# Kernel tuning notes

Measured on AMD Instinct MI355X. Metric: run time of the kernel, lower is better.

Reference implementation:

```python
import jax, jax.numpy as jnp
import numpy as np

T, B, D, H = 128, 256, 1024, 150  # seq_len, batch, input feat, lstm hidden (bidir out = 2H = 300)


def _lstm_dir(x, Wih, Whh, b):
    # x: [T,Bn,in]; Wih: [4H,in]; Whh: [4H,H]; b: [4H]. PyTorch gate order i,f,g,o.
    xW = jnp.einsum('tbi,gi->tbg', x, Wih) + b
    Bn = x.shape[1]
    init = (jnp.zeros((Bn, H), x.dtype), jnp.zeros((Bn, H), x.dtype))
    def step(carry, xg):
        h, c = carry
        g = xg + h @ Whh.T
        i, f, gg, o = jnp.split(g, 4, axis=-1)
        c = jax.nn.sigmoid(f) * c + jax.nn.sigmoid(i) * jnp.tanh(gg)
        h = jax.nn.sigmoid(o) * jnp.tanh(c)
        return (h, c), h
    _, hs = jax.lax.scan(step, init, xW)
    return hs


def _bidir(x, Wih, Whh, b):
    fwd = _lstm_dir(x, Wih[0], Whh[0], b[0])
    bwd = _lstm_dir(x[::-1], Wih[1], Whh[1], b[1])[::-1]
    return jnp.concatenate([fwd, bwd], axis=-1)


def _bilstm2(x, Wih0, Whh0, b0, Wih1, Whh1, b1):
    # 2-layer bidirectional LSTM (eval mode, dropout off)
    h = _bidir(x, Wih0, Whh0, b0)
    return _bidir(h, Wih1, Whh1, b1)


def setup_inputs() -> dict:
    key = jax.random.key(0)
    ks = iter(jax.random.split(key, 32))
    U = jax.random.normal(next(ks), (T, B, D), jnp.float32)
    speaker = jax.random.randint(next(ks), (T, B), 0, 2)
    qmask = jax.nn.one_hot(speaker, 2, dtype=jnp.int32)  # [T,B,2] speaker one-hot
    umask = jnp.ones((T, B), jnp.float32)
    seq_lengths = jnp.full((B,), T, dtype=jnp.int32)
    def w(shape):
        return jax.random.normal(next(ks), shape, jnp.float32) * 0.05
    inp = dict(U=U, qmask=qmask, umask=umask, seq_lengths=seq_lengths)
    for pfx in ('rnn', 'pr'):
        inp[pfx + '_Wih0'] = w((2, 4 * H, D))
        inp[pfx + '_Whh0'] = w((2, 4 * H, H))
        inp[pfx + '_b0'] = w((2, 4 * H))
        inp[pfx + '_Wih1'] = w((2, 4 * H, 2 * H))
        inp[pfx + '_Whh1'] = w((2, 4 * H, H))
        inp[pfx + '_b1'] = w((2, 4 * H))
    return inp


def reference(U, qmask, umask, seq_lengths, rnn_Wih0, rnn_Whh0, rnn_b0, rnn_Wih1, rnn_Whh1, rnn_b1, pr_Wih0, pr_Whh0, pr_b0, pr_Wih1, pr_Whh1, pr_b1):
    speaker = jnp.argmax(qmask, axis=-1)  # [T,B] party id of each utterance
    # position of utterance t within its party's compacted sequence
    pos = jnp.take_along_axis(jnp.cumsum(qmask, axis=0), speaker[..., None], axis=-1)[..., 0] - 1  # [T,B]
    bidx = jnp.broadcast_to(jnp.arange(B)[None, :], (T, B))
    # scatter utterances into per-party sequences: [2,T,B,D]
    U_parties = jnp.zeros((2, T, B, D), U.dtype).at[speaker, pos, bidx].set(U)
    xp = jnp.concatenate([U_parties[0], U_parties[1]], axis=1)  # [T,2B,D]
    Ep = _bilstm2(xp, pr_Wih0, pr_Whh0, pr_b0, pr_Wih1, pr_Whh1, pr_b1)  # [T,2B,2H]
    Ep = jnp.stack([Ep[:, :B], Ep[:, B:]], axis=0)  # [2,T,B,2H]
    U_p = Ep[speaker, pos, bidx]  # gather back to dialogue order, [T,B,2H]
    emotions = _bilstm2(U, rnn_Wih0, rnn_Whh0, rnn_b0, rnn_Wih1, rnn_Whh1, rnn_b1)  # [T,B,2H]
    return (emotions + U_p) * umask[..., None]
```

## Files before the change

kernel.cpp:

```cpp
#include <hip/hip_runtime.h>
#include <hip/hip_bf16.h>
#include <math.h>

#define T_ 128
#define B_ 256
#define BP 512
#define D_ 1024
#define H_ 150
#define G_ 600
#define O_ 300
#define ROWS 16
#define NT_ 38
#define KT_ 5
#define HSTR 168
#define GST 620
#define TPB 512
#define EIT 5
#define NTB 38

typedef float v4f    __attribute__((ext_vector_type(4)));
typedef short bf16x8 __attribute__((ext_vector_type(8)));
typedef float f32x4  __attribute__((ext_vector_type(4)));
typedef unsigned int u32x4 __attribute__((ext_vector_type(4)));
union HU { u32x4 u; bf16x8 h; };

static const size_t N_INV   = 0;
static const size_t N_WPK   = 65536;
static const size_t N_BPK   = N_WPK + 778240;
static const size_t N_HREG  = N_BPK + 2490368;
static const size_t N_X     = N_HREG + 29491200;
static const size_t N_TOTAL = N_X + 78643200 + 256;

static const size_t BPK0_STR = 1245184;
static const size_t BPK1_STR = 389120;

static const size_t INV_OFF   = 0;
static const size_t WIHT0_OFF = 65536;
static const size_t WIHT1_OFF = WIHT0_OFF + 4ull * 1024 * 600;
static const size_t WPK_OFF   = WIHT1_OFF + 4ull * 300 * 600;
static const size_t WPK_WORDS = 8ull * NT_ * KT_ * 2 * 512 / 2;
static const size_t XW_OFF    = WPK_OFF + WPK_WORDS;
static const size_t XSLOT     = 32768ull * 600;
static size_t hrnn_off(int nslots) { return XW_OFF + (size_t)nslots * XSLOT; }
static size_t hpr_off(int nslots)  { return hrnn_off(nslots) + 32768ull * 300; }
static size_t total_words(int nslots) { return hpr_off(nslots) + 65536ull * 300; }

__device__ __forceinline__ float fsig(float x) {
    return __builtin_amdgcn_rcpf(1.f + __expf(-x));
}
__device__ __forceinline__ float ftanh(float x) {
    float xc = fminf(fmaxf(x, -15.f), 15.f);
    float e = __expf(-2.f * xc);
    return (1.f - e) * __builtin_amdgcn_rcpf(1.f + e);
}

__global__ void k_pos(const int* __restrict__ qmask, int* __restrict__ inv) {
    int b = threadIdx.x;
    for (int p = 0; p < T_; ++p) {
        inv[p * BP + b] = -1;
        inv[p * BP + B_ + b] = -1;
    }
    int c0 = 0, c1 = 0;
    for (int t = 0; t < T_; ++t) {
        int s = qmask[(t * B_ + b) * 2 + 1];
        int p = s ? c1++ : c0++;
        inv[p * BP + s * B_ + b] = t * B_ + b;
    }
}

__global__ void k_transpose(const float* __restrict__ src, float* __restrict__ dst,
                            int K) {
    int idx = blockIdx.x * 256 + threadIdx.x;
    int total = K * G_;
    if (idx < total) {
        int k = idx / G_, g = idx - k * G_;
        dst[idx] = src[(size_t)g * K + k];
    }
}

struct PackArgs { const float* whh[8]; };
__global__ void k_pack(PackArgs pa, unsigned short* __restrict__ wpk) {
    int gid = blockIdx.x * 256 + threadIdx.x;
    int lane = gid & 63;
    int q = gid >> 6;
    int kt = q % KT_; q /= KT_;
    int nt = q % NT_; q /= NT_;
    if (q >= 8) return;
    const float* W = pa.whh[q];
    int col = nt * 16 + (lane & 15);
    int kbase = kt * 32 + (lane >> 4) * 8;
    size_t base = ((((size_t)q * NT_ + nt) * KT_ + kt) * 2) * 512 + (size_t)lane * 8;
    for (int j = 0; j < 8; ++j) {
        int k = kbase + j;
        float v = (col < G_ && k < H_) ? W[(size_t)col * H_ + k] : 0.f;
        unsigned u = __float_as_uint(v);
        unsigned short hi = (unsigned short)(u >> 16);
        float hf = __uint_as_float(u & 0xffff0000u);
        unsigned short lo = (unsigned short)(__float_as_uint(v - hf) >> 16);
        wpk[base + j] = hi;
        wpk[base + 512 + j] = lo;
    }
}

__global__ void k_packB(const float* __restrict__ W, int K, int KT,
                        unsigned short* __restrict__ out) {
    int gid = blockIdx.x * 256 + threadIdx.x;
    int lane = gid & 63, q = gid >> 6;
    int kt = q % KT, nt = q / KT;
    if (nt >= NTB) return;
    int col = nt * 16 + (lane & 15);
    int kb = kt * 32 + (lane >> 4) * 8;
    size_t base = ((size_t)(kt * NTB + nt) * 2) * 512 + (size_t)lane * 8;
    bf16x8 h8 = {0, 0, 0, 0, 0, 0, 0, 0};
    bf16x8 l8 = {0, 0, 0, 0, 0, 0, 0, 0};
#pragma unroll
    for (int j = 0; j < 8; ++j) {
        int k = kb + j;
        float v = (col < G_ && k < K) ? W[(size_t)col * K + k] : 0.f;
        unsigned u = __float_as_uint(v);
        h8[j] = (short)(u >> 16);
        float hf = __uint_as_float(u & 0xffff0000u);
        l8[j] = (short)(__float_as_uint(v - hf) >> 16);
    }
    *(bf16x8*)(out + base) = h8;
    *(bf16x8*)(out + base + 512) = l8;
}

__global__ void k_packU(const float* __restrict__ A, unsigned short* __restrict__ hi,
                        unsigned short* __restrict__ lo) {
    int gid = blockIdx.x * 256 + threadIdx.x;
    int kc = gid & 127, rr = gid >> 7;
    const float* ap = A + (size_t)rr * 1024 + kc * 8;
    size_t off = ((size_t)((rr >> 4) * 128 + kc) * 16 + (rr & 15)) * 8;
    bf16x8 h8, l8;
#pragma unroll
    for (int j = 0; j < 8; ++j) {
        float v = ap[j];
        unsigned u = __float_as_uint(v);
        h8[j] = (short)(u >> 16);
        float hf = __uint_as_float(u & 0xffff0000u);
        l8[j] = (short)(__float_as_uint(v - hf) >> 16);
    }
    *(bf16x8*)(hi + off) = h8;
    *(bf16x8*)(lo + off) = l8;
}

__global__ void k_recode(unsigned int* __restrict__ p, int n4) {
    int gid = blockIdx.x * 256 + threadIdx.x;
    if (gid >= n4) return;
    u32x4 w = *(u32x4*)(p + (size_t)gid * 4);
#pragma unroll
    for (int j = 0; j < 4; ++j) {
        unsigned u = w[j];
        float v = __uint_as_float(u);
        float hf = __uint_as_float(u & 0xffff0000u);
        w[j] = (u & 0xffff0000u) | (__float_as_uint(v - hf) >> 16);
    }
    *(u32x4*)(p + (size_t)gid * 4) = w;
}


#define LOADK(kt_, S)                                                          \
  {                                                                            \
    if (MODE == 0) {                                                           \
      _Pragma("unroll") for (int mi = 0; mi < 4; ++mi) {                       \
        size_t aoff = ((size_t)((m0 >> 4) + mi) * KA + (kt_) * 4 + quad);      \
        aoff = (aoff * 16 + col16) * 8;                                        \
        a_h##S[mi] = *(const bf16x8*)(Ahi + aoff);                             \
        a_l##S[mi] = *(const bf16x8*)(Alo + aoff);                             \
      }                                                                        \
    } else {                                                                   \
      _Pragma("unroll") for (int mi = 0; mi < 4; ++mi) {                       \
        const unsigned int* ap =                                               \
            Aw + (size_t)(m0 + mi * 16 + col16) * KA + (kt_) * 32 + quad * 8;  \
        u32x4 w0 = *(const u32x4*)ap;                                          \
        u32x4 w1 = *(const u32x4*)(ap + 4);                                    \
        HU hh, ll;                                                             \
        hh.u.x = (w0.x >> 16) | (w0.y & 0xffff0000u);                          \
        hh.u.y = (w0.z >> 16) | (w0.w & 0xffff0000u);                          \
        hh.u.z = (w1.x >> 16) | (w1.y & 0xffff0000u);                          \
        hh.u.w = (w1.z >> 16) | (w1.w & 0xffff0000u);                          \
        ll.u.x = (w0.x & 0xffffu) | (w0.y << 16);                              \
        ll.u.y = (w0.z & 0xffffu) | (w0.w << 16);                              \
        ll.u.z = (w1.x & 0xffffu) | (w1.y << 16);                              \
        ll.u.w = (w1.z & 0xffffu) | (w1.w << 16);                              \
        a_h##S[mi] = hh.h;                                                     \
        a_l##S[mi] = ll.h;                                                     \
      }                                                                        \
    }                                                                          \
    _Pragma("unroll") for (int ni = 0; ni < 4; ++ni) {                         \
      if (bnv[ni]) {                                                           \
        size_t bo = ((size_t)((kt_) * NTB + nt0 + ni) * 2) * 512 + lane * 8;   \
        b_h##S[ni] = *(const bf16x8*)(Bpk + bo);                               \
        b_l##S[ni] = *(const bf16x8*)(Bpk + bo + 512);                         \
      }                                                                        \
    }                                                                          \
  }

#define MMK(S)                                                                 \
  _Pragma("unroll") for (int mi = 0; mi < 4; ++mi)                             \
    _Pragma("unroll") for (int ni = 0; ni < 4; ++ni) {                         \
      acc[mi][ni] = __builtin_amdgcn_mfma_f32_16x16x32_bf16(                   \
          a_h##S[mi], b_h##S[ni], acc[mi][ni], 0, 0, 0);                       \
      acc[mi][ni] = __builtin_amdgcn_mfma_f32_16x16x32_bf16(                   \
          a_h##S[mi], b_l##S[ni], acc[mi][ni], 0, 0, 0);                       \
      acc[mi][ni] = __builtin_amdgcn_mfma_f32_16x16x32_bf16(                   \
          a_l##S[mi], b_h##S[ni], acc[mi][ni], 0, 0, 0);                       \
    }

template<int MODE, int KTN, int KA>
__global__ __launch_bounds__(256) void k_mgemm(const unsigned short* __restrict__ Ahi,
                                               const unsigned short* __restrict__ Alo,
                                               const unsigned int* __restrict__ Aw,
                                               const unsigned short* __restrict__ Bpk,
                                               const float* __restrict__ bias,
                                               float* __restrict__ C) {
    int tid = threadIdx.x, lane = tid & 63, wv = tid >> 6;
    int col16 = lane & 15, quad = lane >> 4;
    int n0 = blockIdx.x * 128 + (wv & 1) * 64;
    int m0 = blockIdx.y * 128 + (wv >> 1) * 64;
    int nt0 = n0 >> 4;

    bool bnv[4]; float bs[4];
#pragma unroll
    for (int ni = 0; ni < 4; ++ni) {
        int nt = nt0 + ni;
        bnv[ni] = (nt < NTB);
        int cc = nt * 16 + col16;
        bs[ni] = (cc < G_) ? bias[cc] : 0.f;
    }

    f32x4 acc[4][4];
#pragma unroll
    for (int mi = 0; mi < 4; ++mi)
#pragma unroll
        for (int ni = 0; ni < 4; ++ni) acc[mi][ni] = (f32x4){0.f, 0.f, 0.f, 0.f};

    bf16x8 z8 = {0, 0, 0, 0, 0, 0, 0, 0};
    bf16x8 a_h0[4], a_l0[4], b_h0[4], b_l0[4];
    bf16x8 a_h1[4], a_l1[4], b_h1[4], b_l1[4];
#pragma unroll
    for (int ni = 0; ni < 4; ++ni) {
        b_h0[ni] = z8; b_l0[ni] = z8; b_h1[ni] = z8; b_l1[ni] = z8;
    }

    LOADK(0, 0);
#pragma unroll 1
    for (int kt = 0; kt < KTN; kt += 2) {
        LOADK(kt + 1, 1);
        MMK(0);
        if (kt + 2 < KTN) { LOADK(kt + 2, 0); }
        MMK(1);
    }

#pragma unroll
    for (int mi = 0; mi < 4; ++mi)
#pragma unroll
        for (int ni = 0; ni < 4; ++ni) {
            int col = n0 + ni * 16 + col16;
            if (col < G_) {
#pragma unroll
                for (int p = 0; p < 4; ++p)
                    C[(size_t)(m0 + mi * 16 + quad * 4 + p) * G_ + col] =
                        acc[mi][ni][p] + bs[ni];
            }
        }
}

__global__ __launch_bounds__(256) void k_gemm(const float* __restrict__ A,
                                              const float* __restrict__ BT,
                                              const float* __restrict__ bias,
                                              float* __restrict__ C,
                                              int M, int K) {
    __shared__ __align__(16) float As[16][136];
    __shared__ __align__(16) float Bs[16][68];
    int n0 = blockIdx.x * 64, m0 = blockIdx.y * 128;
    int tid = threadIdx.x;
    int tx = tid & 15, ty = tid >> 4;
    int ar = tid >> 2, ac = (tid & 3) * 4;
    int kr = tid >> 4, nc = (tid & 15) * 4;
    float acc[8][4];
#pragma unroll
    for (int i = 0; i < 8; ++i)
#pragma unroll
        for (int j = 0; j < 4; ++j) acc[i][j] = 0.f;

    for (int k0 = 0; k0 < K; k0 += 16) {
        bool fullK = (k0 + 16 <= K);
#pragma unroll
        for (int half = 0; half < 2; ++half) {
            int m = m0 + ar + half * 64;
            const float* ap = A + (size_t)m * K + k0 + ac;
            if (fullK) {
                v4f v = *(const v4f*)ap;
                As[ac + 0][ar + half * 64] = v.x;
                As[ac + 1][ar + half * 64] = v.y;
                As[ac + 2][ar + half * 64] = v.z;
                As[ac + 3][ar + half * 64] = v.w;
            } else {
#pragma unroll
                for (int i = 0; i < 4; ++i) {
                    int k = k0 + ac + i;
                    As[ac + i][ar + half * 64] = (k < K) ? ap[i] : 0.f;
                }
            }
        }
        {
            int k = k0 + kr, n = n0 + nc;
            if (fullK && n + 3 < G_) {
                v4f v = *(const v4f*)(BT + (size_t)k * G_ + n);
                Bs[kr][nc + 0] = v.x; Bs[kr][nc + 1] = v.y;
                Bs[kr][nc + 2] = v.z; Bs[kr][nc + 3] = v.w;
            } else {
#pragma unroll
                for (int i = 0; i < 4; ++i) {
                    int nn = n + i;
                    Bs[kr][nc + i] = (k < K && nn < G_) ? BT[(size_t)k * G_ + nn] : 0.f;
                }
            }
        }
        __syncthreads();
#pragma unroll
        for (int kk = 0; kk < 16; ++kk) {
            v4f a0 = *(const v4f*)&As[kk][ty * 8];
            v4f a1 = *(const v4f*)&As[kk][ty * 8 + 4];
            v4f b  = *(const v4f*)&Bs[kk][tx * 4];
            const float* af = (const float*)&a0;
            const float* af2 = (const float*)&a1;
            const float* bf = (const float*)&b;
#pragma unroll
            for (int i = 0; i < 4; ++i)
#pragma unroll
                for (int j = 0; j < 4; ++j) {
                    acc[i][j] += af[i] * bf[j];
                    acc[4 + i][j] += af2[i] * bf[j];
                }
        }
        __syncthreads();
    }
    int n = n0 + tx * 4;
    if (n + 3 < G_) {
        v4f bv = *(const v4f*)(bias + n);
#pragma unroll
        for (int i = 0; i < 8; ++i) {
            int m = m0 + ty * 8 + i;
            v4f o = {acc[i][0] + bv.x, acc[i][1] + bv.y, acc[i][2] + bv.z, acc[i][3] + bv.w};
            *(v4f*)(C + (size_t)m * G_ + n) = o;
        }
    } else {
#pragma unroll
        for (int i = 0; i < 8; ++i) {
            int m = m0 + ty * 8 + i;
#pragma unroll
            for (int j = 0; j < 4; ++j)
                if (n + j < G_) C[(size_t)m * G_ + n + j] = acc[i][j] + bias[n + j];
        }
    }
}

struct Combo {
    const float* xw;
    const unsigned short* wpk;
    const float* bias;
    float* out;
    int Bn, colOff, bwd, gIn, gOut;
};
struct ScanArgs {
    Combo c[4];
    const int* inv;
    const float* addSrc;
    const float* umask;
    int blkStart[5];
};

__global__ __launch_bounds__(TPB) void k_scan(ScanArgs args) {
    int bx = blockIdx.x, ci = 0;
#pragma unroll
    for (int i = 1; i < 4; ++i)
        if (bx >= args.blkStart[i]) ci = i;
    Combo cb = args.c[ci];
    int row0 = (bx - args.blkStart[ci]) * ROWS;

    __shared__ __align__(16) unsigned short hsh[ROWS * HSTR];
    __shared__ __align__(16) unsigned short hsl[ROWS * HSTR];
    __shared__ float cs[ROWS * 152];
    __shared__ float gs[ROWS * GST];
    int tid = threadIdx.x;
    int lane = tid & 63, wv = tid >> 6;
    int col16 = lane & 15, quad = lane >> 4;
    for (int i = tid; i < ROWS * HSTR; i += TPB) { hsh[i] = 0; hsl[i] = 0; }
    for (int i = tid; i < ROWS * 152; i += TPB) cs[i] = 0.f;
    __syncthreads();

    int er[EIT], ej[EIT];
#pragma unroll
    for (int it = 0; it < EIT; ++it) {
        int i = tid + it * TPB;
        er[it] = i / 160;
        ej[it] = i - er[it] * 160;
    }

    for (int s = 0; s < T_; ++s) {
        int t = cb.bwd ? (T_ - 1 - s) : s;

        float xi[EIT], xf_[EIT], xg[EIT], xo[EIT];
#pragma unroll
        for (int it = 0; it < EIT; ++it) {
            int r = er[it], j = ej[it];
            const float* xr;
            if (cb.gIn) {
                int g = args.inv[t * cb.Bn + row0 + r];
                xr = (g >= 0) ? cb.xw + (size_t)g * G_ : cb.bias;
            } else {
                xr = cb.xw + ((size_t)t * cb.Bn + row0 + r) * G_;
            }
            bool act = (j < H_);
            xi[it]  = act ? xr[j] : 0.f;
            xf_[it] = act ? xr[H_ + j] : 0.f;
            xg[it]  = act ? xr[2 * H_ + j] : 0.f;
            xo[it]  = act ? xr[3 * H_ + j] : 0.f;
        }

        bf16x8 ahi[KT_], alo[KT_];
#pragma unroll
        for (int kt = 0; kt < KT_; ++kt) {
            int off = col16 * HSTR + kt * 32 + quad * 8;
            ahi[kt] = *(const bf16x8*)&hsh[off];
            alo[kt] = *(const bf16x8*)&hsl[off];
        }

        for (int nt = wv; nt < NT_; nt += 8) {
            f32x4 a0 = {0.f, 0.f, 0.f, 0.f};
            f32x4 a1 = {0.f, 0.f, 0.f, 0.f};
            const bf16x8* bp = (const bf16x8*)cb.wpk + ((size_t)nt * KT_) * 2 * 64 + lane;
#pragma unroll
            for (int kt = 0; kt < KT_; ++kt) {
                bf16x8 bhi = bp[0];
                bf16x8 blo = bp[64];
                bp += 128;
                if (kt < 3) {
                    a0 = __builtin_amdgcn_mfma_f32_16x16x32_bf16(ahi[kt], bhi, a0, 0, 0, 0);
                    a0 = __builtin_amdgcn_mfma_f32_16x16x32_bf16(ahi[kt], blo, a0, 0, 0, 0);
                    a0 = __builtin_amdgcn_mfma_f32_16x16x32_bf16(alo[kt], bhi, a0, 0, 0, 0);
                } else {
                    a1 = __builtin_amdgcn_mfma_f32_16x16x32_bf16(ahi[kt], bhi, a1, 0, 0, 0);
                    a1 = __builtin_amdgcn_mfma_f32_16x16x32_bf16(ahi[kt], blo, a1, 0, 0, 0);
                    a1 = __builtin_amdgcn_mfma_f32_16x16x32_bf16(alo[kt], bhi, a1, 0, 0, 0);
                }
            }
            f32x4 acc = a0 + a1;
#pragma unroll
            for (int p = 0; p < 4; ++p)
                gs[(quad * 4 + p) * GST + nt * 16 + col16] = acc[p];
        }
        __syncthreads();

#pragma unroll
        for (int it = 0; it < EIT; ++it) {
            int r = er[it], j = ej[it];
            if (j < H_) {
                float gi = gs[r * GST + j] + xi[it];
                float gf = gs[r * GST + H_ + j] + xf_[it];
                float gg = gs[r * GST + 2 * H_ + j] + xg[it];
                float go = gs[r * GST + 3 * H_ + j] + xo[it];
                float ii = fsig(gi), ff = fsig(gf), oo = fsig(go);
                float cc = ff * cs[r * 152 + j] + ii * ftanh(gg);
                float hh = oo * ftanh(cc);
                cs[r * 152 + j] = cc;
                unsigned u = __float_as_uint(hh);
                hsh[r * HSTR + j] = (unsigned short)(u >> 16);
                float hf = __uint_as_float(u & 0xffff0000u);
                hsl[r * HSTR + j] = (unsigned short)(__float_as_uint(hh - hf) >> 16);
                if (cb.gOut) {
                    int g = args.inv[t * cb.Bn + row0 + r];
                    if (g >= 0) {
                        size_t o = (size_t)g * O_ + cb.colOff + j;
                        if (args.addSrc)
                            cb.out[o] = (args.addSrc[o] + hh) * args.umask[g];
                        else
                            cb.out[o] = hh;
                    }
                } else {
                    cb.out[((size_t)t * cb.Bn + row0 + r) * O_ + cb.colOff + j] = hh;
                }
            }
        }
        __syncthreads();
    }
}

extern "C" void kernel_launch(void* const* d_in, const int* in_sizes, int n_in,
                              void* d_out, int out_size, void* d_ws, size_t ws_size,
                              hipStream_t stream) {
    const float* U        = (const float*)d_in[0];
    const int*   qmask    = (const int*)d_in[1];
    const float* umask    = (const float*)d_in[2];
    const float* rnn_Wih0 = (const float*)d_in[4];
    const float* rnn_Whh0 = (const float*)d_in[5];
    const float* rnn_b0   = (const float*)d_in[6];
    const float* rnn_Wih1 = (const float*)d_in[7];
    const float* rnn_Whh1 = (const float*)d_in[8];
    const float* rnn_b1   = (const float*)d_in[9];
    const float* pr_Wih0  = (const float*)d_in[10];
    const float* pr_Whh0  = (const float*)d_in[11];
    const float* pr_b0    = (const float*)d_in[12];
    const float* pr_Wih1  = (const float*)d_in[13];
    const float* pr_Whh1  = (const float*)d_in[14];
    const float* pr_b1    = (const float*)d_in[15];

    float* ws = (float*)d_ws;
    dim3 blk(256);
    dim3 sblk(TPB);
    const int INF = 0x7fffffff;

    const size_t WPS = (size_t)NT_ * KT_ * 2 * 512;

    ScanArgs z = {};
    auto setCombo = [&](ScanArgs& sa, int i, const float* xw, unsigned short* wbase,
                        int wslot, const float* bi, float* o, int Bn, int co, int bw,
                        int gi, int go) {
        sa.c[i].xw = xw; sa.c[i].wpk = wbase + (size_t)wslot * WPS;
        sa.c[i].bias = bi; sa.c[i].out = o;
        sa.c[i].Bn = Bn; sa.c[i].colOff = co; sa.c[i].bwd = bw;
        sa.c[i].gIn = gi; sa.c[i].gOut = go;
    };

    PackArgs pa;
    for (int d = 0; d < 2; ++d) {
        pa.whh[0 + d] = rnn_Whh0 + (size_t)d * G_ * H_;
        pa.whh[2 + d] = pr_Whh0  + (size_t)d * G_ * H_;
        pa.whh[4 + d] = rnn_Whh1 + (size_t)d * G_ * H_;
        pa.whh[6 + d] = pr_Whh1  + (size_t)d * G_ * H_;
    }
    int packLanes = 8 * NT_ * KT_ * 64;

    if (ws_size >= N_TOTAL * 4ull) {
        int*   inv   = (int*)d_ws + N_INV;
        unsigned short* wpk = (unsigned short*)(ws + N_WPK);
        unsigned short* bpk = (unsigned short*)(ws + N_BPK);
        float* h_rnn = ws + N_HREG;
        float* h_pr  = h_rnn + 32768ull * 300;
        unsigned short* Uhi = (unsigned short*)h_rnn;
        unsigned short* Ulo = Uhi + 16384ull * 1024;
        float* X[4];
        for (int i = 0; i < 4; ++i) X[i] = ws + N_X + (size_t)i * 19660800ull;

        k_pos<<<dim3(1), dim3(256), 0, stream>>>(qmask, inv);
        k_pack<<<dim3((packLanes + 255) / 256), dim3(256), 0, stream>>>(pa, wpk);

        const float* W0p[4] = {rnn_Wih0, rnn_Wih0 + (size_t)G_ * D_,
                               pr_Wih0,  pr_Wih0 + (size_t)G_ * D_};
        const float* b0p[4] = {rnn_b0, rnn_b0 + G_, pr_b0, pr_b0 + G_};
        {
            int lanes = 32 * NTB * 64;
            for (int g = 0; g < 4; ++g)
                k_packB<<<dim3((lanes + 255) / 256), blk, 0, stream>>>(
                    W0p[g], D_, 32, bpk + (size_t)g * BPK0_STR);
        }

        dim3 gm0(5, 128);
        for (int half = 0; half < 2; ++half) {
            k_packU<<<dim3(8192), blk, 0, stream>>>(U + (size_t)half * 16384 * D_, Uhi, Ulo);
            for (int g = 0; g < 4; ++g)
                k_mgemm<0, 32, 128><<<gm0, blk, 0, stream>>>(
                    Uhi, Ulo, nullptr, bpk + (size_t)g * BPK0_STR, b0p[g],
                    X[g] + (size_t)half * 16384 * G_);
        }

        ScanArgs sa = z;
        sa.inv = inv;
        setCombo(sa, 0, X[0], wpk, 0, nullptr, h_rnn, B_, 0, 0, 0, 0);
        setCombo(sa, 1, X[1], wpk, 1, nullptr, h_rnn, B_, H_, 1, 0, 0);
        setCombo(sa, 2, X[2], wpk, 2, pr_b0 + 0 * G_, h_pr, BP, 0, 0, 1, 0);
        setCombo(sa, 3, X[3], wpk, 3, pr_b0 + 1 * G_, h_pr, BP, H_, 1, 1, 0);
        sa.blkStart[0] = 0; sa.blkStart[1] = 16; sa.blkStart[2] = 32;
        sa.blkStart[3] = 64; sa.blkStart[4] = 96;
        k_scan<<<dim3(96), sblk, 0, stream>>>(sa);

        k_recode<<<dim3((2457600 + 255) / 256), blk, 0, stream>>>((unsigned int*)h_rnn, 2457600);
        k_recode<<<dim3((4915200 + 255) / 256), blk, 0, stream>>>((unsigned int*)h_pr, 4915200);
        const float* W1p[4] = {rnn_Wih1, rnn_Wih1 + (size_t)G_ * O_,
                               pr_Wih1,  pr_Wih1 + (size_t)G_ * O_};
        {
            int lanes = 10 * NTB * 64;
            for (int g = 0; g < 4; ++g)
                k_packB<<<dim3((lanes + 255) / 256), blk, 0, stream>>>(
                    W1p[g], O_, 10, bpk + (size_t)g * BPK1_STR);
        }

        dim3 gm1r(5, 256), gm1p(5, 512);
        k_mgemm<1, 10, 300><<<gm1r, blk, 0, stream>>>(
            nullptr, nullptr, (unsigned int*)h_rnn, bpk + 0 * BPK1_STR, rnn_b1 + 0 * G_, X[0]);
        k_mgemm<1, 10, 300><<<gm1r, blk, 0, stream>>>(
            nullptr, nullptr, (unsigned int*)h_rnn, bpk + 1 * BPK1_STR, rnn_b1 + 1 * G_, X[1]);
        k_mgemm<1, 10, 300><<<gm1p, blk, 0, stream>>>(
            nullptr, nullptr, (unsigned int*)h_pr, bpk + 2 * BPK1_STR, pr_b1 + 0 * G_, X[2]);
        ScanArgs sr = z;
        sr.inv = inv;
        setCombo(sr, 0, X[0], wpk, 4, nullptr, h_rnn, B_, 0, 0, 0, 0);
        setCombo(sr, 1, X[1], wpk, 5, nullptr, h_rnn, B_, H_, 1, 0, 0);
        sr.blkStart[0] = 0; sr.blkStart[1] = 16; sr.blkStart[2] = INF;
        sr.blkStart[3] = INF; sr.blkStart[4] = 32;
        k_scan<<<dim3(32), sblk, 0, stream>>>(sr);

        k_mgemm<1, 10, 300><<<gm1p, blk, 0, stream>>>(
            nullptr, nullptr, (unsigned int*)h_pr, bpk + 3 * BPK1_STR, pr_b1 + 1 * G_, X[0]);
        ScanArgs sp = z;
        sp.inv = inv; sp.addSrc = h_rnn; sp.umask = umask;
        setCombo(sp, 0, X[2], wpk, 6, nullptr, (float*)d_out, BP, 0, 0, 0, 1);
        setCombo(sp, 1, X[0], wpk, 7, nullptr, (float*)d_out, BP, H_, 1, 0, 1);
        sp.blkStart[0] = 0; sp.blkStart[1] = 32; sp.blkStart[2] = INF;
        sp.blkStart[3] = INF; sp.blkStart[4] = 64;
        k_scan<<<dim3(64), sblk, 0, stream>>>(sp);
        return;
    }

    int*   inv   = (int*)d_ws + INV_OFF;
    float* wihT0 = ws + WIHT0_OFF;
    float* wihT1 = ws + WIHT1_OFF;
    unsigned short* wpk = (unsigned short*)(ws + WPK_OFF);
    float* X0    = ws + XW_OFF;
    float* X1    = X0 + XSLOT;
    float* h_rnn = ws + hrnn_off(2);
    float* h_pr  = ws + hpr_off(2);

    const size_t W0S = 1024ull * 600, W1S = 300ull * 600;

    k_pos<<<dim3(1), dim3(256), 0, stream>>>(qmask, inv);
    auto TP = [&](const float* src, float* dst, int K) {
        int total = K * G_;
        k_transpose<<<dim3((total + 255) / 256), dim3(256), 0, stream>>>(src, dst, K);
    };
    for (int d = 0; d < 2; ++d) {
        TP(rnn_Wih0 + (size_t)d * G_ * D_, wihT0 + (0 + d) * W0S, D_);
        TP(pr_Wih0  + (size_t)d * G_ * D_, wihT0 + (2 + d) * W0S, D_);
        TP(rnn_Wih1 + (size_t)d * G_ * O_, wihT1 + (0 + d) * W1S, O_);
        TP(pr_Wih1  + (size_t)d * G_ * O_, wihT1 + (2 + d) * W1S, O_);
    }
    k_pack<<<dim3((packLanes + 255) / 256), dim3(256), 0, stream>>>(pa, wpk);

    dim3 g32k(10, 256), g64k(10, 512);
    for (int d = 0; d < 2; ++d) {
        k_gemm<<<g32k, blk, 0, stream>>>(U, wihT0 + (0 + d) * W0S, rnn_b0 + d * G_, X0, 32768, D_);
        k_gemm<<<g32k, blk, 0, stream>>>(U, wihT0 + (2 + d) * W0S, pr_b0 + d * G_, X1, 32768, D_);
        ScanArgs sa = z;
        sa.inv = inv;
        setCombo(sa, 0, X0, wpk, 0 + d, nullptr, h_rnn, B_, d * H_, d, 0, 0);
        setCombo(sa, 1, X1, wpk, 2 + d, pr_b0 + d * G_, h_pr, BP, d * H_, d, 1, 0);
        sa.blkStart[0] = 0; sa.blkStart[1] = 16; sa.blkStart[2] = INF;
        sa.blkStart[3] = INF; sa.blkStart[4] = 48;
        k_scan<<<dim3(48), sblk, 0, stream>>>(sa);
    }
    k_gemm<<<g32k, blk, 0, stream>>>(h_rnn, wihT1 + 0 * W1S, rnn_b1 + 0 * G_, X0, 32768, O_);
    k_gemm<<<g32k, blk, 0, stream>>>(h_rnn, wihT1 + 1 * W1S, rnn_b1 + 1 * G_, X1, 32768, O_);
    {
        ScanArgs sr = z;
        sr.inv = inv;
        setCombo(sr, 0, X0, wpk, 4, nullptr, h_rnn, B_, 0, 0, 0, 0);
        setCombo(sr, 1, X1, wpk, 5, nullptr, h_rnn, B_, H_, 1, 0, 0);
        sr.blkStart[0] = 0; sr.blkStart[1] = 16; sr.blkStart[2] = INF;
        sr.blkStart[3] = INF; sr.blkStart[4] = 32;
        k_scan<<<dim3(32), sblk, 0, stream>>>(sr);
    }
    for (int d = 0; d < 2; ++d) {
        k_gemm<<<g64k, blk, 0, stream>>>(h_pr, wihT1 + (2 + d) * W1S, pr_b1 + d * G_, X0, 65536, O_);
        ScanArgs sp = z;
        sp.inv = inv; sp.addSrc = h_rnn; sp.umask = umask;
        setCombo(sp, 0, X0, wpk, 6 + d, nullptr, (float*)d_out, BP, d * H_, d, 0, 1);
        sp.blkStart[0] = 0; sp.blkStart[1] = INF; sp.blkStart[2] = INF;
        sp.blkStart[3] = INF; sp.blkStart[4] = 32;
        k_scan<<<dim3(32), sblk, 0, stream>>>(sp);
    }
}
```

Measured before the change: 4.103 ms.

## Fuse layer-1 input projection into recurrent scan and run all four layer-1 scans concurrently

Layer 0 now writes its hidden states straight into a packed bf16 hi/lo MFMA operand layout, so the separate recode pass goes away. Layer 1 no longer runs a separate input-projection GEMM. Each timestep of the new scan kernel computes x·Wih with MFMA alongside h·Whh. This lets all four layer-1 direction/stack scans run in one 96-block launch instead of two serialized launches, and the final residual add plus mask becomes a separate elementwise kernel. The trade-off is extra per-step MFMA and global loads of Wih inside the latency-bound recurrence, plus a zeroing pass over the packed buffer.

```diff
diff --git a/kernel.cpp b/kernel.cpp
--- a/kernel.cpp
+++ b/kernel.cpp
@@ -12,6 +12,8 @@
 #define ROWS 16
 #define NT_ 38
 #define KT_ 5
+#define KTX 10
+#define KAP 40
 #define HSTR 168
 #define GST 620
 #define TPB 512
@@ -26,13 +28,16 @@
 
 static const size_t N_INV   = 0;
 static const size_t N_WPK   = 65536;
-static const size_t N_BPK   = N_WPK + 778240;
-static const size_t N_HREG  = N_BPK + 2490368;
-static const size_t N_X     = N_HREG + 29491200;
+static const size_t N_BW1   = N_WPK + 778240;
+static const size_t N_HPK   = N_BW1 + 778240;
+static const size_t N_X     = N_HPK + 31457280;
 static const size_t N_TOTAL = N_X + 78643200 + 256;
 
-static const size_t BPK0_STR = 1245184;
-static const size_t BPK1_STR = 389120;
+static const size_t WPS      = (size_t)NT_ * KT_ * 2 * 512;
+static const size_t BW1_STR  = (size_t)KTX * NTB * 2 * 512;
+static const size_t BW0_STR  = 32ull * NTB * 2 * 512;
+static const size_t RNN_PL   = 2048ull * KAP * 128;
+static const size_t PR_PL    = 4096ull * KAP * 128;
 
 static const size_t INV_OFF   = 0;
 static const size_t WIHT0_OFF = 65536;
@@ -43,7 +48,6 @@
 static const size_t XSLOT     = 32768ull * 600;
 static size_t hrnn_off(int nslots) { return XW_OFF + (size_t)nslots * XSLOT; }
 static size_t hpr_off(int nslots)  { return hrnn_off(nslots) + 32768ull * 300; }
-static size_t total_words(int nslots) { return hpr_off(nslots) + 65536ull * 300; }
 
 __device__ __forceinline__ float fsig(float x) {
     return __builtin_amdgcn_rcpf(1.f + __expf(-x));
@@ -66,6 +70,11 @@
         int p = s ? c1++ : c0++;
         inv[p * BP + s * B_ + b] = t * B_ + b;
     }
+}
+
+__global__ void k_zero(unsigned int* __restrict__ p, int n4) {
+    int gid = blockIdx.x * 256 + threadIdx.x;
+    if (gid < n4) *(u32x4*)(p + (size_t)gid * 4) = (u32x4){0, 0, 0, 0};
 }
 
 __global__ void k_transpose(const float* __restrict__ src, float* __restrict__ dst,
@@ -144,21 +153,6 @@
     *(bf16x8*)(hi + off) = h8;
     *(bf16x8*)(lo + off) = l8;
 }
-
-__global__ void k_recode(unsigned int* __restrict__ p, int n4) {
-    int gid = blockIdx.x * 256 + threadIdx.x;
-    if (gid >= n4) return;
-    u32x4 w = *(u32x4*)(p + (size_t)gid * 4);
-#pragma unroll
-    for (int j = 0; j < 4; ++j) {
-        unsigned u = w[j];
-        float v = __uint_as_float(u);
-        float hf = __uint_as_float(u & 0xffff0000u);
-        w[j] = (u & 0xffff0000u) | (__float_as_uint(v - hf) >> 16);
-    }
-    *(u32x4*)(p + (size_t)gid * 4) = w;
-}
-
 
 #define LOADK(kt_, S)                                                          \
   {                                                                            \
@@ -358,6 +352,269 @@
     }
 }
 
+struct Combo0 {
+    const float* xw;
+    const unsigned short* wpk;
+    const float* bias;
+    unsigned short* phi;
+    unsigned short* plo;
+    int Bn, colOff, bwd, gIn;
+};
+struct Scan0Args { Combo0 c[4]; const int* inv; int blkStart[5]; };
+
+__global__ __launch_bounds__(TPB) void k_scan0(Scan0Args args) {
+    int bx = blockIdx.x, ci = 0;
+#pragma unroll
+    for (int i = 1; i < 4; ++i)
+        if (bx >= args.blkStart[i]) ci = i;
+    Combo0 cb = args.c[ci];
+    int row0 = (bx - args.blkStart[ci]) * ROWS;
+
+    __shared__ __align__(16) unsigned short hsh[ROWS * HSTR];
+    __shared__ __align__(16) unsigned short hsl[ROWS * HSTR];
+    __shared__ float cs[ROWS * 152];
+    __shared__ float gs[ROWS * GST];
+    int tid = threadIdx.x;
+    int lane = tid & 63, wv = tid >> 6;
+    int col16 = lane & 15, quad = lane >> 4;
+    for (int i = tid; i < ROWS * HSTR; i += TPB) { hsh[i] = 0; hsl[i] = 0; }
+    for (int i = tid; i < ROWS * 152; i += TPB) cs[i] = 0.f;
+    __syncthreads();
+
+    int er[EIT], ej[EIT];
+#pragma unroll
+    for (int it = 0; it < EIT; ++it) {
+        int i = tid + it * TPB;
+        er[it] = i / 160;
+        ej[it] = i - er[it] * 160;
+    }
+
+    for (int s = 0; s < T_; ++s) {
+        int t = cb.bwd ? (T_ - 1 - s) : s;
+
+        float xi[EIT], xf_[EIT], xg[EIT], xo[EIT];
+#pragma unroll
+        for (int it = 0; it < EIT; ++it) {
+            int r = er[it], j = ej[it];
+            const float* xr;
+            if (cb.gIn) {
+                int g = args.inv[t * cb.Bn + row0 + r];
+                xr = (g >= 0) ? cb.xw + (size_t)g * G_ : cb.bias;
+            } else {
+                xr = cb.xw + ((size_t)t * cb.Bn + row0 + r) * G_;
+            }
+            bool act = (j < H_);
+            xi[it]  = act ? xr[j] : 0.f;
+            xf_[it] = act ? xr[H_ + j] : 0.f;
+            xg[it]  = act ? xr[2 * H_ + j] : 0.f;
+            xo[it]  = act ? xr[3 * H_ + j] : 0.f;
+        }
+
+        bf16x8 ahi[KT_], alo[KT_];
+#pragma unroll
+        for (int kt = 0; kt < KT_; ++kt) {
+            int off = col16 * HSTR + kt * 32 + quad * 8;
+            ahi[kt] = *(const bf16x8*)&hsh[off];
+            alo[kt] = *(const bf16x8*)&hsl[off];
+        }
+
+        for (int nt = wv; nt < NT_; nt += 8) {
+            f32x4 a0 = {0.f, 0.f, 0.f, 0.f};
+            f32x4 a1 = {0.f, 0.f, 0.f, 0.f};
+            const bf16x8* bp = (const bf16x8*)cb.wpk + ((size_t)nt * KT_) * 2 * 64 + lane;
+#pragma unroll
+            for (int kt = 0; kt < KT_; ++kt) {
+                bf16x8 bhi = bp[0];
+                bf16x8 blo = bp[64];
+                bp += 128;
+                if (kt < 3) {
+                    a0 = __builtin_amdgcn_mfma_f32_16x16x32_bf16(ahi[kt], bhi, a0, 0, 0, 0);
+                    a0 = __builtin_amdgcn_mfma_f32_16x16x32_bf16(ahi[kt], blo, a0, 0, 0, 0);
+                    a0 = __builtin_amdgcn_mfma_f32_16x16x32_bf16(alo[kt], bhi, a0, 0, 0, 0);
+                } else {
+                    a1 = __builtin_amdgcn_mfma_f32_16x16x32_bf16(ahi[kt], bhi, a1, 0, 0, 0);
+                    a1 = __builtin_amdgcn_mfma_f32_16x16x32_bf16(ahi[kt], blo, a1, 0, 0, 0);
+                    a1 = __builtin_amdgcn_mfma_f32_16x16x32_bf16(alo[kt], bhi, a1, 0, 0, 0);
+                }
+            }
+            f32x4 acc = a0 + a1;
+#pragma unroll
+            for (int p = 0; p < 4; ++p)
+                gs[(quad * 4 + p) * GST + nt * 16 + col16] = acc[p];
+        }
+        __syncthreads();
+
+        size_t mb = ((size_t)t * cb.Bn + row0) >> 4;
+#pragma unroll
+        for (int it = 0; it < EIT; ++it) {
+            int r = er[it], j = ej[it];
+            if (j < H_) {
+                float gi = gs[r * GST + j] + xi[it];
+                float gf = gs[r * GST + H_ + j] + xf_[it];
+                float gg = gs[r * GST + 2 * H_ + j] + xg[it];
+                float go = gs[r * GST + 3 * H_ + j] + xo[it];
+                float ii = fsig(gi), ff = fsig(gf), oo = fsig(go);
+                float cc = ff * cs[r * 152 + j] + ii * ftanh(gg);
+                float hh = oo * ftanh(cc);
+                cs[r * 152 + j] = cc;
+                unsigned u = __float_as_uint(hh);
+                unsigned short hi16 = (unsigned short)(u >> 16);
+                float hf = __uint_as_float(u & 0xffff0000u);
+                unsigned short lo16 = (unsigned short)(__float_as_uint(hh - hf) >> 16);
+                hsh[r * HSTR + j] = hi16;
+                hsl[r * HSTR + j] = lo16;
+                int k = cb.colOff + j;
+                size_t off = (mb * KAP + (k >> 3)) * 128 + (size_t)r * 8 + (k & 7);
+                cb.phi[off] = hi16;
+                cb.plo[off] = lo16;
+            }
+        }
+        __syncthreads();
+    }
+}
+
+struct Combo1 {
+    const unsigned short* xphi;
+    const unsigned short* xplo;
+    const unsigned short* whh;
+    const unsigned short* wih;
+    const float* bias;
+    float* out;
+    int Bn, colOff, bwd, gOut;
+};
+struct Scan1Args { Combo1 c[4]; const int* inv; int blkStart[5]; };
+
+__global__ __launch_bounds__(TPB) void k_scan1(Scan1Args args) {
+    int bx = blockIdx.x, ci = 0;
+#pragma unroll
+    for (int i = 1; i < 4; ++i)
+        if (bx >= args.blkStart[i]) ci = i;
+    Combo1 cb = args.c[ci];
+    int row0 = (bx - args.blkStart[ci]) * ROWS;
+
+    __shared__ __align__(16) unsigned short hsh[ROWS * HSTR];
+    __shared__ __align__(16) unsigned short hsl[ROWS * HSTR];
+    __shared__ float cs[ROWS * 152];
+    __shared__ float gs[ROWS * GST];
+    int tid = threadIdx.x;
+    int lane = tid & 63, wv = tid >> 6;
+    int col16 = lane & 15, quad = lane >> 4;
+    for (int i = tid; i < ROWS * HSTR; i += TPB) { hsh[i] = 0; hsl[i] = 0; }
+    for (int i = tid; i < ROWS * 152; i += TPB) cs[i] = 0.f;
+    __syncthreads();
+
+    int er[EIT], ej[EIT];
+    float bxi[EIT], bxf[EIT], bxg[EIT], bxo[EIT];
+#pragma unroll
+    for (int it = 0; it < EIT; ++it) {
+        int i = tid + it * TPB;
+        er[it] = i / 160;
+        ej[it] = i - er[it] * 160;
+        int j = ej[it];
+        bool act = (j < H_);
+        bxi[it] = act ? cb.bias[j] : 0.f;
+        bxf[it] = act ? cb.bias[H_ + j] : 0.f;
+        bxg[it] = act ? cb.bias[2 * H_ + j] : 0.f;
+        bxo[it] = act ? cb.bias[3 * H_ + j] : 0.f;
+    }
+
+    for (int s = 0; s < T_; ++s) {
+        int t = cb.bwd ? (T_ - 1 - s) : s;
+        size_t mb = ((size_t)t * cb.Bn + row0) >> 4;
+
+        bf16x8 xh[KTX], xl[KTX];
+#pragma unroll
+        for (int kt = 0; kt < KTX; ++kt) {
+            size_t off = (mb * KAP + kt * 4 + quad) * 128 + (size_t)col16 * 8;
+            xh[kt] = *(const bf16x8*)(cb.xphi + off);
+            xl[kt] = *(const bf16x8*)(cb.xplo + off);
+        }
+
+        bf16x8 ahi[KT_], alo[KT_];
+#pragma unroll
+        for (int kt = 0; kt < KT_; ++kt) {
+            int off = col16 * HSTR + kt * 32 + quad * 8;
+            ahi[kt] = *(const bf16x8*)&hsh[off];
+            alo[kt] = *(const bf16x8*)&hsl[off];
+        }
+
+        for (int nt = wv; nt < NT_; nt += 8) {
+            f32x4 a0 = {0.f, 0.f, 0.f, 0.f};
+            f32x4 a1 = {0.f, 0.f, 0.f, 0.f};
+            const bf16x8* bp = (const bf16x8*)cb.whh + ((size_t)nt * KT_) * 2 * 64 + lane;
+#pragma unroll
+            for (int kt = 0; kt < KT_; ++kt) {
+                bf16x8 bhi = bp[0];
+                bf16x8 blo = bp[64];
+                bp += 128;
+                if (kt < 3) {
+                    a0 = __builtin_amdgcn_mfma_f32_16x16x32_bf16(ahi[kt], bhi, a0, 0, 0, 0);
+                    a0 = __builtin_amdgcn_mfma_f32_16x16x32_bf16(ahi[kt], blo, a0, 0, 0, 0);
+                    a0 = __builtin_amdgcn_mfma_f32_16x16x32_bf16(alo[kt], bhi, a0, 0, 0, 0);
+                } else {
+                    a1 = __builtin_amdgcn_mfma_f32_16x16x32_bf16(ahi[kt], bhi, a1, 0, 0, 0);
+                    a1 = __builtin_amdgcn_mfma_f32_16x16x32_bf16(ahi[kt], blo, a1, 0, 0, 0);
+                    a1 = __builtin_amdgcn_mfma_f32_16x16x32_bf16(alo[kt], bhi, a1, 0, 0, 0);
+                }
+            }
+#pragma unroll
+            for (int kt = 0; kt < KTX; ++kt) {
+                const bf16x8* xp = (const bf16x8*)cb.wih + ((size_t)(kt * NTB + nt) * 2) * 64 + lane;
+                bf16x8 bhi = xp[0];
+                bf16x8 blo = xp[64];
+                if (kt & 1) {
+                    a1 = __builtin_amdgcn_mfma_f32_16x16x32_bf16(xh[kt], bhi, a1, 0, 0, 0);
+                    a1 = __builtin_amdgcn_mfma_f32_16x16x32_bf16(xh[kt], blo, a1, 0, 0, 0);
+                    a1 = __builtin_amdgcn_mfma_f32_16x16x32_bf16(xl[kt], bhi, a1, 0, 0, 0);
+                } else {
+                    a0 = __builtin_amdgcn_mfma_f32_16x16x32_bf16(xh[kt], bhi, a0, 0, 0, 0);
+                    a0 = __builtin_amdgcn_mfma_f32_16x16x32_bf16(xh[kt], blo, a0, 0, 0, 0);
+                    a0 = __builtin_amdgcn_mfma_f32_16x16x32_bf16(xl[kt], bhi, a0, 0, 0, 0);
+                }
+            }
+            f32x4 acc = a0 + a1;
+#pragma unroll
+            for (int p = 0; p < 4; ++p)
+                gs[(quad * 4 + p) * GST + nt * 16 + col16] = acc[p];
+        }
+        __syncthreads();
+
+#pragma unroll
+        for (int it = 0; it < EIT; ++it) {
+            int r = er[it], j = ej[it];
+            if (j < H_) {
+                float gi = gs[r * GST + j] + bxi[it];
+                float gf = gs[r * GST + H_ + j] + bxf[it];
+                float gg = gs[r * GST + 2 * H_ + j] + bxg[it];
+                float go = gs[r * GST + 3 * H_ + j] + bxo[it];
+                float ii = fsig(gi), ff = fsig(gf), oo = fsig(go);
+                float cc = ff * cs[r * 152 + j] + ii * ftanh(gg);
+                float hh = oo * ftanh(cc);
+                cs[r * 152 + j] = cc;
+                unsigned u = __float_as_uint(hh);
+                hsh[r * HSTR + j] = (unsigned short)(u >> 16);
+                float hf = __uint_as_float(u & 0xffff0000u);
+                hsl[r * HSTR + j] = (unsigned short)(__float_as_uint(hh - hf) >> 16);
+                if (cb.gOut) {
+                    int g = args.inv[t * cb.Bn + row0 + r];
+                    if (g >= 0)
+                        cb.out[(size_t)g * O_ + cb.colOff + j] = hh;
+                } else {
+                    cb.out[((size_t)t * cb.Bn + row0 + r) * O_ + cb.colOff + j] = hh;
+                }
+            }
+        }
+        __syncthreads();
+    }
+}
+
+__global__ void k_add(float* __restrict__ out, const float* __restrict__ up,
+                      const float* __restrict__ um) {
+    int idx = blockIdx.x * 256 + threadIdx.x;
+    if (idx < T_ * B_ * O_)
+        out[idx] = (out[idx] + up[idx]) * um[idx / O_];
+}
+
 struct Combo {
     const float* xw;
     const unsigned short* wpk;
@@ -513,18 +770,6 @@
     dim3 sblk(TPB);
     const int INF = 0x7fffffff;
 
-    const size_t WPS = (size_t)NT_ * KT_ * 2 * 512;
-
-    ScanArgs z = {};
-    auto setCombo = [&](ScanArgs& sa, int i, const float* xw, unsigned short* wbase,
-                        int wslot, const float* bi, float* o, int Bn, int co, int bw,
-                        int gi, int go) {
-        sa.c[i].xw = xw; sa.c[i].wpk = wbase + (size_t)wslot * WPS;
-        sa.c[i].bias = bi; sa.c[i].out = o;
-        sa.c[i].Bn = Bn; sa.c[i].colOff = co; sa.c[i].bwd = bw;
-        sa.c[i].gIn = gi; sa.c[i].gOut = go;
-    };
-
     PackArgs pa;
     for (int d = 0; d < 2; ++d) {
         pa.whh[0 + d] = rnn_Whh0 + (size_t)d * G_ * H_;
@@ -537,16 +782,30 @@
     if (ws_size >= N_TOTAL * 4ull) {
         int*   inv   = (int*)d_ws + N_INV;
         unsigned short* wpk = (unsigned short*)(ws + N_WPK);
-        unsigned short* bpk = (unsigned short*)(ws + N_BPK);
-        float* h_rnn = ws + N_HREG;
-        float* h_pr  = h_rnn + 32768ull * 300;
-        unsigned short* Uhi = (unsigned short*)h_rnn;
-        unsigned short* Ulo = Uhi + 16384ull * 1024;
+        unsigned short* bw1 = (unsigned short*)(ws + N_BW1);
+        unsigned short* hpk = (unsigned short*)(ws + N_HPK);
+        unsigned short* rnnHi = hpk;
+        unsigned short* rnnLo = rnnHi + RNN_PL;
+        unsigned short* prHi  = rnnLo + RNN_PL;
+        unsigned short* prLo  = prHi + PR_PL;
+        unsigned short* bw0 = hpk;
+        unsigned short* Uhi = hpk + 4 * BW0_STR;
+        unsigned short* Ulo = Uhi + 16777216ull;
         float* X[4];
         for (int i = 0; i < 4; ++i) X[i] = ws + N_X + (size_t)i * 19660800ull;
+        float* Uptmp = X[0];
 
         k_pos<<<dim3(1), dim3(256), 0, stream>>>(qmask, inv);
         k_pack<<<dim3((packLanes + 255) / 256), dim3(256), 0, stream>>>(pa, wpk);
+
+        const float* W1p[4] = {rnn_Wih1, rnn_Wih1 + (size_t)G_ * O_,
+                               pr_Wih1,  pr_Wih1 + (size_t)G_ * O_};
+        {
+            int lanes = KTX * NTB * 64;
+            for (int g = 0; g < 4; ++g)
+                k_packB<<<dim3((lanes + 255) / 256), blk, 0, stream>>>(
+                    W1p[g], O_, KTX, bw1 + (size_t)g * BW1_STR);
+        }
 
         const float* W0p[4] = {rnn_Wih0, rnn_Wih0 + (size_t)G_ * D_,
                                pr_Wih0,  pr_Wih0 + (size_t)G_ * D_};
@@ -555,7 +814,7 @@
             int lanes = 32 * NTB * 64;
             for (int g = 0; g < 4; ++g)
                 k_packB<<<dim3((lanes + 255) / 256), blk, 0, stream>>>(
-                    W0p[g], D_, 32, bpk + (size_t)g * BPK0_STR);
+                    W0p[g], D_, 32, bw0 + (size_t)g * BW0_STR);
         }
 
         dim3 gm0(5, 128);
@@ -563,55 +822,51 @@
             k_packU<<<dim3(8192), blk, 0, stream>>>(U + (size_t)half * 16384 * D_, Uhi, Ulo);
             for (int g = 0; g < 4; ++g)
                 k_mgemm<0, 32, 128><<<gm0, blk, 0, stream>>>(
-                    Uhi, Ulo, nullptr, bpk + (size_t)g * BPK0_STR, b0p[g],
+                    Uhi, Ulo, nullptr, bw0 + (size_t)g * BW0_STR, b0p[g],
                     X[g] + (size_t)half * 16384 * G_);
         }
 
-        ScanArgs sa = z;
+        k_zero<<<dim3((31457280 / 4 + 255) / 256), blk, 0, stream>>>(
+            (unsigned int*)hpk, 31457280 / 4);
+
+        Scan0Args sa = {};
         sa.inv = inv;
-        setCombo(sa, 0, X[0], wpk, 0, nullptr, h_rnn, B_, 0, 0, 0, 0);
-        setCombo(sa, 1, X[1], wpk, 1, nullptr, h_rnn, B_, H_, 1, 0, 0);
-        setCombo(sa, 2, X[2], wpk, 2, pr_b0 + 0 * G_, h_pr, BP, 0, 0, 1, 0);
-        setCombo(sa, 3, X[3], wpk, 3, pr_b0 + 1 * G_, h_pr, BP, H_, 1, 1, 0);
+        auto set0 = [&](int i, const float* xw, int wslot, const float* bi,
+                        unsigned short* phi, unsigned short* plo,
+                        int Bn, int co, int bw, int gi) {
+            sa.c[i].xw = xw; sa.c[i].wpk = wpk + (size_t)wslot * WPS;
+            sa.c[i].bias = bi; sa.c[i].phi = phi; sa.c[i].plo = plo;
+            sa.c[i].Bn = Bn; sa.c[i].colOff = co; sa.c[i].bwd = bw; sa.c[i].gIn = gi;
+        };
+        set0(0, X[0], 0, nullptr, rnnHi, rnnLo, B_, 0, 0, 0);
+        set0(1, X[1], 1, nullptr, rnnHi, rnnLo, B_, H_, 1, 0);
+        set0(2, X[2], 2, pr_b0 + 0 * G_, prHi, prLo, BP, 0, 0, 1);
+        set0(3, X[3], 3, pr_b0 + 1 * G_, prHi, prLo, BP, H_, 1, 1);
         sa.blkStart[0] = 0; sa.blkStart[1] = 16; sa.blkStart[2] = 32;
         sa.blkStart[3] = 64; sa.blkStart[4] = 96;
-        k_scan<<<dim3(96), sblk, 0, stream>>>(sa);
-
-        k_recode<<<dim3((2457600 + 255) / 256), blk, 0, stream>>>((unsigned int*)h_rnn, 2457600);
-        k_recode<<<dim3((4915200 + 255) / 256), blk, 0, stream>>>((unsigned int*)h_pr, 4915200);
-        const float* W1p[4] = {rnn_Wih1, rnn_Wih1 + (size_t)G_ * O_,
-                               pr_Wih1,  pr_Wih1 + (size_t)G_ * O_};
-        {
-            int lanes = 10 * NTB * 64;
-            for (int g = 0; g < 4; ++g)
-                k_packB<<<dim3((lanes + 255) / 256), blk, 0, stream>>>(
-                    W1p[g], O_, 10, bpk + (size_t)g * BPK1_STR);
-        }
-
-        dim3 gm1r(5, 256), gm1p(5, 512);
-        k_mgemm<1, 10, 300><<<gm1r, blk, 0, stream>>>(
-            nullptr, nullptr, (unsigned int*)h_rnn, bpk + 0 * BPK1_STR, rnn_b1 + 0 * G_, X[0]);
-        k_mgemm<1, 10, 300><<<gm1r, blk, 0, stream>>>(
-            nullptr, nullptr, (unsigned int*)h_rnn, bpk + 1 * BPK1_STR, rnn_b1 + 1 * G_, X[1]);
-        k_mgemm<1, 10, 300><<<gm1p, blk, 0, stream>>>(
-            nullptr, nullptr, (unsigned int*)h_pr, bpk + 2 * BPK1_STR, pr_b1 + 0 * G_, X[2]);
-        ScanArgs sr = z;
-        sr.inv = inv;
-        setCombo(sr, 0, X[0], wpk, 4, nullptr, h_rnn, B_, 0, 0, 0, 0);
-        setCombo(sr, 1, X[1], wpk, 5, nullptr, h_rnn, B_, H_, 1, 0, 0);
-        sr.blkStart[0] = 0; sr.blkStart[1] = 16; sr.blkStart[2] = INF;
-        sr.blkStart[3] = INF; sr.blkStart[4] = 32;
-        k_scan<<<dim3(32), sblk, 0, stream>>>(sr);
-
-        k_mgemm<1, 10, 300><<<gm1p, blk, 0, stream>>>(
-            nullptr, nullptr, (unsigned int*)h_pr, bpk + 3 * BPK1_STR, pr_b1 + 1 * G_, X[0]);
-        ScanArgs sp = z;
-        sp.inv = inv; sp.addSrc = h_rnn; sp.umask = umask;
-        setCombo(sp, 0, X[2], wpk, 6, nullptr, (float*)d_out, BP, 0, 0, 0, 1);
-        setCombo(sp, 1, X[0], wpk, 7, nullptr, (float*)d_out, BP, H_, 1, 0, 1);
-        sp.blkStart[0] = 0; sp.blkStart[1] = 32; sp.blkStart[2] = INF;
-        sp.blkStart[3] = INF; sp.blkStart[4] = 64;
-        k_scan<<<dim3(64), sblk, 0, stream>>>(sp);
+        k_scan0<<<dim3(96), sblk, 0, stream>>>(sa);
+
+        Scan1Args sm = {};
+        sm.inv = inv;
+        auto set1 = [&](int i, const unsigned short* xh, const unsigned short* xl,
+                        int wslot, int bslot, const float* bi, float* o,
+                        int Bn, int co, int bw, int go) {
+            sm.c[i].xphi = xh; sm.c[i].xplo = xl;
+            sm.c[i].whh = wpk + (size_t)wslot * WPS;
+            sm.c[i].wih = bw1 + (size_t)bslot * BW1_STR;
+            sm.c[i].bias = bi; sm.c[i].out = o;
+            sm.c[i].Bn = Bn; sm.c[i].colOff = co; sm.c[i].bwd = bw; sm.c[i].gOut = go;
+        };
+        set1(0, rnnHi, rnnLo, 4, 0, rnn_b1 + 0 * G_, (float*)d_out, B_, 0, 0, 0);
+        set1(1, rnnHi, rnnLo, 5, 1, rnn_b1 + 1 * G_, (float*)d_out, B_, H_, 1, 0);
+        set1(2, prHi, prLo, 6, 2, pr_b1 + 0 * G_, Uptmp, BP, 0, 0, 1);
+        set1(3, prHi, prLo, 7, 3, pr_b1 + 1 * G_, Uptmp, BP, H_, 1, 1);
+        sm.blkStart[0] = 0; sm.blkStart[1] = 16; sm.blkStart[2] = 32;
+        sm.blkStart[3] = 64; sm.blkStart[4] = 96;
+        k_scan1<<<dim3(96), sblk, 0, stream>>>(sm);
+
+        k_add<<<dim3((T_ * B_ * O_ + 255) / 256), dim3(256), 0, stream>>>(
+            (float*)d_out, Uptmp, umask);
         return;
     }
 
@@ -639,14 +894,24 @@
     }
     k_pack<<<dim3((packLanes + 255) / 256), dim3(256), 0, stream>>>(pa, wpk);
 
+    ScanArgs z = {};
+    auto setCombo = [&](ScanArgs& s2, int i, const float* xw, int wslot,
+                        const float* bi, float* o, int Bn, int co, int bw,
+                        int gi, int go) {
+        s2.c[i].xw = xw; s2.c[i].wpk = wpk + (size_t)wslot * WPS;
+        s2.c[i].bias = bi; s2.c[i].out = o;
+        s2.c[i].Bn = Bn; s2.c[i].colOff = co; s2.c[i].bwd = bw;
+        s2.c[i].gIn = gi; s2.c[i].gOut = go;
+    };
+
     dim3 g32k(10, 256), g64k(10, 512);
     for (int d = 0; d < 2; ++d) {
         k_gemm<<<g32k, blk, 0, stream>>>(U, wihT0 + (0 + d) * W0S, rnn_b0 + d * G_, X0, 32768, D_);
         k_gemm<<<g32k, blk, 0, stream>>>(U, wihT0 + (2 + d) * W0S, pr_b0 + d * G_, X1, 32768, D_);
         ScanArgs sa = z;
         sa.inv = inv;
-        setCombo(sa, 0, X0, wpk, 0 + d, nullptr, h_rnn, B_, d * H_, d, 0, 0);
-        setCombo(sa, 1, X1, wpk, 2 + d, pr_b0 + d * G_, h_pr, BP, d * H_, d, 1, 0);
+        setCombo(sa, 0, X0, 0 + d, nullptr, h_rnn, B_, d * H_, d, 0, 0);
+        setCombo(sa, 1, X1, 2 + d, pr_b0 + d * G_, h_pr, BP, d * H_, d, 1, 0);
         sa.blkStart[0] = 0; sa.blkStart[1] = 16; sa.blkStart[2] = INF;
         sa.blkStart[3] = INF; sa.blkStart[4] = 48;
         k_scan<<<dim3(48), sblk, 0, stream>>>(sa);
@@ -656,8 +921,8 @@
     {
         ScanArgs sr = z;
         sr.inv = inv;
-        setCombo(sr, 0, X0, wpk, 4, nullptr, h_rnn, B_, 0, 0, 0, 0);
-        setCombo(sr, 1, X1, wpk, 5, nullptr, h_rnn, B_, H_, 1, 0, 0);
+        setCombo(sr, 0, X0, 4, nullptr, h_rnn, B_, 0, 0, 0, 0);
+        setCombo(sr, 1, X1, 5, nullptr, h_rnn, B_, H_, 1, 0, 0);
         sr.blkStart[0] = 0; sr.blkStart[1] = 16; sr.blkStart[2] = INF;
         sr.blkStart[3] = INF; sr.blkStart[4] = 32;
         k_scan<<<dim3(32), sblk, 0, stream>>>(sr);
@@ -666,7 +931,7 @@
         k_gemm<<<g64k, blk, 0, stream>>>(h_pr, wihT1 + (2 + d) * W1S, pr_b1 + d * G_, X0, 65536, O_);
         ScanArgs sp = z;
         sp.inv = inv; sp.addSrc = h_rnn; sp.umask = umask;
-        setCombo(sp, 0, X0, wpk, 6 + d, nullptr, (float*)d_out, BP, d * H_, d, 0, 1);
+        setCombo(sp, 0, X0, 6 + d, nullptr, (float*)d_out, BP, d * H_, d, 0, 1);
         sp.blkStart[0] = 0; sp.blkStart[1] = INF; sp.blkStart[2] = INF;
         sp.blkStart[3] = INF; sp.blkStart[4] = 32;
         k_scan<<<dim3(32), sblk, 0, stream>>>(sp);
```

Result: slower. 5.464 ms (+33.2%).
